# Optimization experiments

Hardware: AMD Instinct MI355X
Metric: run time of the kernel (lower is better)

## Reference

```python
import jax, jax.numpy as jnp
import numpy as np
import math

# Single graph (batch vector identically 0): per-graph topk and global_max_pool
# reduce to static lax.top_k and jnp.max. Pooled edge_index from SAGPooling is
# discarded because KnnEdges rebuilds the graph every layer (no_op=False).
N = 20000      # nodes
HID = 128      # in_channels == hidden_channels
L = 3          # num_layers
RATIO = 0.5    # pool_ratio
K0, KINC = 6, 2  # KnnEdges start_k / k_increment
OUT = 5


def setup_inputs() -> dict:
    key = jax.random.key(0)
    ks = jax.random.split(key, 10)
    s = 0.05  # keep tanh scores unsaturated
    x = jax.random.normal(ks[0], (N, HID), jnp.float32)
    pos = jax.random.uniform(ks[1], (N, 2), jnp.float32) * 100.0
    src = jax.random.randint(ks[2], (N * K0,), 0, N)
    dst = jnp.repeat(jnp.arange(N), K0)
    edge_index = jnp.stack([src, dst]).astype(jnp.int32)  # [2, E], row0=src(j), row1=dst(i)
    return dict(
        x=x, pos=pos, edge_index=edge_index,
        Wrel=jax.random.normal(ks[3], (L, HID, HID), jnp.float32) * s,
        brel=jnp.zeros((L, HID), jnp.float32),
        Wroot=jax.random.normal(ks[4], (L, HID, HID), jnp.float32) * s,
        Wprel=jax.random.normal(ks[5], (L, HID), jnp.float32) * s,
        bprel=jnp.zeros((L,), jnp.float32),
        Wproot=jax.random.normal(ks[6], (L, HID), jnp.float32) * s,
        W1=jax.random.normal(ks[7], (HID * L, HID), jnp.float32) * s,
        b1=jnp.zeros((HID,), jnp.float32),
        W2=jax.random.normal(ks[8], (HID, OUT), jnp.float32) * s,
        b2=jnp.zeros((OUT,), jnp.float32),
    )


def _mean_agg(x, src, dst, n):
    # mean over incoming messages x_j for each target i (PyG aggr='mean'; 0 if isolated)
    ssum = jax.ops.segment_sum(x[src], dst, num_segments=n)
    deg = jax.ops.segment_sum(jnp.ones(src.shape, x.dtype), dst, num_segments=n)
    return ssum / jnp.maximum(deg, 1.0)[:, None]


def reference(x, pos, edge_index, Wrel, brel, Wroot, Wprel, bprel, Wproot, W1, b1, W2, b2):
    src, dst = edge_index[0], edge_index[1]
    n = x.shape[0]
    xs = []
    for i in range(L):
        # GraphConv(aggr='mean'): out_i = W_rel @ mean_j x_j + W_root @ x_i + b
        agg = _mean_agg(x, src, dst, n)
        x = jax.nn.relu(agg @ Wrel[i] + x @ Wroot[i] + brel[i])
        # SAGPooling: score GNN = GraphConv(hid->1, aggr='add'); tanh nonlinearity
        sagg = jax.ops.segment_sum(x[src], dst, num_segments=n)
        score = jnp.tanh(sagg @ Wprel[i] + x @ Wproot[i] + bprel[i])  # [n]
        k_keep = math.ceil(RATIO * n)
        vals, perm = jax.lax.top_k(score, k_keep)
        x = x[perm] * vals[:, None]
        xs.append(jnp.max(x, axis=0))  # global_max_pool (single graph)
        # KnnEdges: pos = pos[perm]; rebuild KNN graph with k = start_k + i*k_increment
        pos = pos[perm]
        n = k_keep
        k = K0 + KINC * i
        d2 = jnp.sum((pos[:, None, :] - pos[None, :, :]) ** 2, axis=-1)  # [n, n]
        d2 = jnp.where(jnp.eye(n, dtype=bool), jnp.inf, d2)  # loop=False
        _, nbr = jax.lax.top_k(-d2, k)  # [n, k] nearest neighbors
        src = nbr.reshape(-1)                 # neighbor j (source)
        dst = jnp.repeat(jnp.arange(n), k)    # query i (target)
    h = jnp.concatenate(xs)  # JumpingKnowledge mode='cat' -> [HID*L]
    h = jax.nn.relu(h @ W1 + b1)  # dropout p=0.5 in eval mode: identity
    return (h @ W2 + b2)[None, :]  # [1, OUT]
```

## Files before the change

### kernel.cpp

```cpp
#include <hip/hip_runtime.h>
#include <hip/hip_bf16.h>
#include <math.h>

#define HID 128
#define PR 20
#define CRPB 32
#define CAND_CAP 8192
#define MAXCELLS 4096

__device__ inline int wave_iscan(int v, int lane) {
#pragma unroll
  for (int off = 1; off < 64; off <<= 1) {
    int o = __shfl_up(v, off, 64);
    if (lane >= off) v += o;
  }
  return v;
}

template <int K>
__global__ __launch_bounds__(256) void k_conv_fused(
    const float* __restrict__ x, const int* __restrict__ src, int n, float invk,
    const float* __restrict__ Wrel, const float* __restrict__ Wroot,
    const float* __restrict__ brel,
    const float* __restrict__ wprel, const float* __restrict__ wproot,
    float* __restrict__ out, float* __restrict__ uo, float* __restrict__ vo) {
  __shared__ float4 sagg4[CRPB][HID / 4];
  __shared__ float4 sx4[CRPB][HID / 4];
  __shared__ int ssrc[CRPB * K];
  int t = threadIdx.x;
  int i0 = blockIdx.x * CRPB;
  const int nK = n * K;
  for (int s = t; s < CRPB * K; s += 256) {
    int gi = i0 * K + s;
    int v = (gi < nK) ? src[gi] : 0;
    ssrc[s] = ((unsigned)v < (unsigned)n) ? v : 0;
  }
  __syncthreads();
  {
    int fq = t & 31, h = t >> 5;
    const float4* x4 = (const float4*)x;
    for (int r = h; r < CRPB; r += 8) {
      int row = i0 + r;
      float4 s = make_float4(0.f, 0.f, 0.f, 0.f);
      float4 xv = make_float4(0.f, 0.f, 0.f, 0.f);
      if (row < n) {
#pragma unroll
        for (int j = 0; j < K; ++j) {
          float4 xx = x4[(size_t)ssrc[r * K + j] * 32 + fq];
          s.x += xx.x; s.y += xx.y; s.z += xx.z; s.w += xx.w;
        }
        xv = x4[(size_t)row * 32 + fq];
      }
      s.x *= invk; s.y *= invk; s.z *= invk; s.w *= invk;
      sagg4[r][fq] = s;
      sx4[r][fq] = xv;
    }
  }
  __syncthreads();
  int q = t & 31, rg = t >> 5;
  const float4* Wrel4  = (const float4*)Wrel;
  const float4* Wroot4 = (const float4*)Wroot;
  float4 bq = ((const float4*)brel)[q];
  float4 acc[4];
#pragma unroll
  for (int rr = 0; rr < 4; ++rr) acc[rr] = bq;
  int rbase = rg * 4;
#pragma unroll 2
  for (int cq = 0; cq < HID / 4; ++cq) {
    float4 w1[4], w2[4];
#pragma unroll
    for (int uu = 0; uu < 4; ++uu) {
      w1[uu] = Wrel4[(cq * 4 + uu) * 32 + q];
      w2[uu] = Wroot4[(cq * 4 + uu) * 32 + q];
    }
#pragma unroll
    for (int rr = 0; rr < 4; ++rr) {
      float4 a  = sagg4[rbase + rr][cq];
      float4 xx = sx4[rbase + rr][cq];
      acc[rr].x += a.x*w1[0].x + a.y*w1[1].x + a.z*w1[2].x + a.w*w1[3].x
                 + xx.x*w2[0].x + xx.y*w2[1].x + xx.z*w2[2].x + xx.w*w2[3].x;
      acc[rr].y += a.x*w1[0].y + a.y*w1[1].y + a.z*w1[2].y + a.w*w1[3].y
                 + xx.x*w2[0].y + xx.y*w2[1].y + xx.z*w2[2].y + xx.w*w2[3].y;
      acc[rr].z += a.x*w1[0].z + a.y*w1[1].z + a.z*w1[2].z + a.w*w1[3].z
                 + xx.x*w2[0].z + xx.y*w2[1].z + xx.z*w2[2].z + xx.w*w2[3].z;
      acc[rr].w += a.x*w1[0].w + a.y*w1[1].w + a.z*w1[2].w + a.w*w1[3].w
                 + xx.x*w2[0].w + xx.y*w2[1].w + xx.z*w2[2].w + xx.w*w2[3].w;
    }
  }
  float4 wplq = ((const float4*)wprel)[q];
  float4 wprq = ((const float4*)wproot)[q];
#pragma unroll
  for (int rr = 0; rr < 4; ++rr) {
    int row = i0 + rbase + rr;
    float4 v = acc[rr];
    v.x = v.x > 0.f ? v.x : 0.f;
    v.y = v.y > 0.f ? v.y : 0.f;
    v.z = v.z > 0.f ? v.z : 0.f;
    v.w = v.w > 0.f ? v.w : 0.f;
    float pu = 0.f, pv = 0.f;
    if (row < n) {
      ((float4*)out)[(size_t)row * 32 + q] = v;
      pu = v.x * wplq.x + v.y * wplq.y + v.z * wplq.z + v.w * wplq.w;
      pv = v.x * wprq.x + v.y * wprq.y + v.z * wprq.z + v.w * wprq.w;
    }
#pragma unroll
    for (int o = 16; o; o >>= 1) {
      pu += __shfl_down(pu, o, 32);
      pv += __shfl_down(pv, o, 32);
    }
    if (q == 0 && row < n) { uo[row] = pu; vo[row] = pv; }
  }
}

template <int K>
__global__ __launch_bounds__(256) void k_score_lite(
    const float* __restrict__ u, const float* __restrict__ v,
    const int* __restrict__ src, const float* __restrict__ bprel,
    int n, float* __restrict__ score, unsigned* __restrict__ key,
    unsigned* __restrict__ ghist) {
  __shared__ unsigned lh[1024];
  int t = threadIdx.x;
#pragma unroll
  for (int uu = 0; uu < 4; ++uu) lh[t + uu * 256] = 0u;
  __syncthreads();
  int i = blockIdx.x * 256 + t;
  if (i < n) {
    float s = v[i] + bprel[0];
#pragma unroll
    for (int j = 0; j < K; ++j) s += u[src[i * K + j]];
    float sc = tanhf(s);
    score[i] = sc;
    unsigned bb = __float_as_uint(sc);
    unsigned k2 = (bb & 0x80000000u) ? ~bb : (bb | 0x80000000u);
    key[i] = k2;
    atomicAdd(&lh[k2 >> 22], 1u);
  }
  __syncthreads();
#pragma unroll
  for (int uu = 0; uu < 4; ++uu) {
    unsigned vv = lh[t + uu * 256];
    if (vv) atomicAdd(&ghist[t + uu * 256], vv);
  }
}

__global__ __launch_bounds__(256) void k_collect(
    const unsigned* __restrict__ key, int n, int kk,
    const unsigned* __restrict__ ghist,
    unsigned* __restrict__ BA, unsigned long long* __restrict__ candbuf,
    int* __restrict__ candCnt) {
  __shared__ int wt[4];
  __shared__ unsigned shB, shAbove;
  int t = threadIdx.x;
  int lane = t & 63, wid = t >> 6;
  unsigned h[4]; int s = 0;
#pragma unroll
  for (int uu = 0; uu < 4; ++uu) { h[uu] = ghist[t * 4 + uu]; s += (int)h[uu]; }
  int is = wave_iscan(s, lane);
  if (lane == 63) wt[wid] = is;
  __syncthreads();
  int b = 0, tot = 0;
#pragma unroll
  for (int w2 = 0; w2 < 4; ++w2) { int ss = wt[w2]; if (w2 < wid) b += ss; tot += ss; }
  int c = b + is - s;
#pragma unroll
  for (int uu = 0; uu < 4; ++uu) {
    c += (int)h[uu];
    unsigned above_strict = (unsigned)(tot - c);
    unsigned above_incl = above_strict + h[uu];
    if (above_incl >= (unsigned)kk && above_strict < (unsigned)kk) {
      shB = (unsigned)(t * 4 + uu);
      shAbove = above_strict;
    }
  }
  __syncthreads();
  unsigned B = shB;
  if (blockIdx.x == 0 && t == 0) { BA[0] = B; BA[1] = shAbove; }
  int i = blockIdx.x * 256 + t;
  unsigned long long lmask = (1ull << lane) - 1ull;
  unsigned kv = (i < n) ? key[i] : 0u;
  bool m = (i < n) && ((kv >> 22) == B);
  unsigned long long mm = __ballot(m);
  if (mm) {
    int leader = (int)(__ffsll((long long)mm) - 1);
    int base = 0;
    if (lane == leader) base = atomicAdd(candCnt, (int)__popcll(mm));
    base = __shfl(base, leader, 64);
    if (m) {
      int p = base + (int)__popcll(mm & lmask);
      if (p < CAND_CAP) candbuf[p] = ((unsigned long long)kv << 32) | (unsigned)(~i);
    }
  }
}

__global__ __launch_bounds__(1024) void k_refine(
    const unsigned long long* __restrict__ candbuf, const int* __restrict__ candCnt,
    const unsigned* __restrict__ BA, int kk, unsigned long long* __restrict__ T64) {
  extern __shared__ unsigned long long cands[];
  __shared__ unsigned hist256[256];
  __shared__ unsigned long long sh_prefix;
  __shared__ unsigned sh_remain;
  __shared__ int wtB[4];
  int t = threadIdx.x;
  int lane = t & 63, wid = t >> 6;
  unsigned B = BA[0], above = BA[1];
  int cnt = *candCnt; if (cnt > CAND_CAP) cnt = CAND_CAP;
  for (int i = t; i < cnt; i += 1024) cands[i] = candbuf[i];
  if (t == 0) {
    sh_prefix = ((unsigned long long)B) << 54;
    sh_remain = (unsigned)(kk - (int)above);
  }
  __syncthreads();
  const int shifts[7] = {46, 38, 30, 22, 14, 6, 0};
  for (int p = 0; p < 7; ++p) {
    int shift = shifts[p];
    int bits = (p == 6) ? 6 : 8;
    unsigned mask = (1u << bits) - 1u;
    unsigned long long himask = (p == 0) ? (~0ull << 54)
                                         : (~0ull << (shifts[p - 1]));
    unsigned long long prefix = sh_prefix;
    unsigned rem = sh_remain;
    if (t < 256) hist256[t] = 0u;
    __syncthreads();
    for (int i = t; i < cnt; i += 1024) {
      unsigned long long cc = cands[i];
      if ((cc & himask) == prefix)
        atomicAdd(&hist256[(unsigned)((cc >> shift) & mask)], 1u);
    }
    __syncthreads();
    int hv = (t < 256) ? (int)hist256[t] : 0;
    int iv = wave_iscan(hv, lane);
    if (t < 256 && lane == 63) wtB[wid] = iv;
    __syncthreads();
    if (t < 256) {
      int b = 0, tot = 0;
#pragma unroll
      for (int w2 = 0; w2 < 4; ++w2) { int s = wtB[w2]; if (w2 < wid) b += s; tot += s; }
      unsigned val = (unsigned)(iv + b);
      unsigned sstrict = (unsigned)tot - val;
      if ((unsigned)t <= mask && sstrict < rem && sstrict + (unsigned)hv >= rem) {
        sh_prefix = prefix | ((unsigned long long)t << shift);
        sh_remain = rem - sstrict;
      }
    }
    __syncthreads();
  }
  if (t == 0) T64[0] = sh_prefix;
}

__global__ void k_sel(const unsigned* __restrict__ key, int n,
                      const unsigned long long* __restrict__ T64,
                      int* __restrict__ perm, int* __restrict__ cntSel) {
  int i = blockIdx.x * blockDim.x + threadIdx.x;
  int lane = threadIdx.x & 63;
  unsigned long long lmask = (1ull << lane) - 1ull;
  unsigned long long T = T64[0];
  bool g = false;
  if (i < n) {
    unsigned long long k64 = ((unsigned long long)key[i] << 32) | (unsigned)(~i);
    g = (k64 >= T);
  }
  unsigned long long mg = __ballot(g);
  if (mg) {
    int leader = (int)(__ffsll((long long)mg) - 1);
    int base = 0;
    if (lane == leader) base = atomicAdd(cntSel, (int)__popcll(mg));
    base = __shfl(base, leader, 64);
    if (g) perm[base + (int)__popcll(mg & lmask)] = i;
  }
}

template <int R>
__global__ __launch_bounds__(256) void k_pool_pmax(
    const float* __restrict__ x, const float* __restrict__ score,
    const int* __restrict__ perm, const float* __restrict__ pos_in,
    float* __restrict__ xout, float* __restrict__ pos_out, int store,
    float* __restrict__ pmax, int* __restrict__ counts, int Gg, float inv_w) {
  __shared__ float sm[2][HID];
  int f = threadIdx.x & 127;
  int half = threadIdx.x >> 7;
  int j0 = blockIdx.x * R;
  float mx = -1e30f;
  for (int r = half; r < R; r += 2) {
    int j = j0 + r;
    int node = perm[j];
    float v = score[node];
    float val = x[(size_t)node * HID + f] * v;
    if (store) {
      xout[(size_t)j * HID + f] = val;
      if (f == 0) {
        float px = pos_in[node * 2], py = pos_in[node * 2 + 1];
        pos_out[j * 2] = px; pos_out[j * 2 + 1] = py;
        int cx = min(Gg - 1, max(0, (int)(px * inv_w)));
        int cy = min(Gg - 1, max(0, (int)(py * inv_w)));
        atomicAdd(&counts[cy * Gg + cx], 1);
      }
    }
    mx = fmaxf(mx, val);
  }
  sm[half][f] = mx;
  __syncthreads();
  if (half == 0) pmax[blockIdx.x * HID + f] = fmaxf(sm[0][f], sm[1][f]);
}

__global__ __launch_bounds__(256) void k_scatterF(
    const float2* __restrict__ pos, int m, int Gg, int cells, float inv_w,
    const int* __restrict__ counts, int* __restrict__ startsg, int* __restrict__ zcur,
    float2* __restrict__ spos, int* __restrict__ sidx) {
  __shared__ int sstarts[MAXCELLS];
  __shared__ int wsum[4];
  int t = threadIdx.x;
  int lane = t & 63, wid = t >> 6;
  int base16 = t * 16;
  int c0[16]; int s = 0;
#pragma unroll
  for (int u = 0; u < 16; ++u) {
    int idx = base16 + u;
    c0[u] = (idx < cells) ? counts[idx] : 0;
    s += c0[u];
  }
  int is = wave_iscan(s, lane);
  if (lane == 63) wsum[wid] = is;
  __syncthreads();
  int b = 0;
#pragma unroll
  for (int w2 = 0; w2 < 4; ++w2) { if (w2 < wid) b += wsum[w2]; }
  int excl = b + is - s;
#pragma unroll
  for (int u = 0; u < 16; ++u) {
    int idx = base16 + u;
    if (idx < cells) { sstarts[idx] = excl; excl += c0[u]; }
  }
  __syncthreads();
  if (blockIdx.x == 0) {
    for (int c = t; c < cells; c += 256) startsg[c] = sstarts[c];
  }
  int i = blockIdx.x * 256 + t;
  if (i < m) {
    float2 p = pos[i];
    int cx = min(Gg - 1, max(0, (int)(p.x * inv_w)));
    int cy = min(Gg - 1, max(0, (int)(p.y * inv_w)));
    int cell = cy * Gg + cx;
    int pp = sstarts[cell] + atomicAdd(&zcur[cell], 1);
    spos[pp] = p;
    sidx[pp] = i;
  }
}

template <int K>
__global__ __launch_bounds__(256) void k_knn_wave(const float2* __restrict__ spos,
                           const int* __restrict__ sidx,
                           const int* __restrict__ starts, const int* __restrict__ counts,
                           int m, int G, float w, float inv_w, int* __restrict__ src_out) {
  int lane = threadIdx.x & 63;
  int j = blockIdx.x * (blockDim.x >> 6) + (threadIdx.x >> 6);
  if (j >= m) return;
  float2 qp = spos[j];
  int q = sidx[j];
  int cx = min(G - 1, max(0, (int)(qp.x * inv_w)));
  int cy = min(G - 1, max(0, (int)(qp.y * inv_w)));

  float bd[K]; int bi[K];
#pragma unroll
  for (int t = 0; t < K; ++t) { bd[t] = 1e30f; bi[t] = 0; }

  auto scan_span = [&](int s, int e) {
    for (int p = s + lane; p < e; p += 64) {
      if (p == j) continue;
      float2 pp = spos[p];
      float dx = qp.x - pp.x, dy = qp.y - pp.y;
      float d = dx * dx + dy * dy;
      if (d < bd[K - 1]) {
        float dd = d; int ii = sidx[p];
#pragma unroll
        for (int t = 0; t < K; ++t) {
          bool sw = dd < bd[t];
          float od = bd[t]; int oi = bi[t];
          if (sw) { bd[t] = dd; bi[t] = ii; dd = od; ii = oi; }
        }
      }
    }
  };

  {
    int xl = max(0, cx - 1), xh = min(G - 1, cx + 1);
    int y0 = max(0, cy - 1), y1 = min(G - 1, cy + 1);
    int ss[3], ee[3]; int nr = 0;
    for (int y = y0; y <= y1; ++y) {
      int b = y * G;
      ss[nr] = starts[b + xl];
      ee[nr] = starts[b + xh] + counts[b + xh];
      ++nr;
    }
    for (int t = 0; t < nr; ++t) scan_span(ss[t], ee[t]);
  }

  int r = 1;
  unsigned long long mg[K];
  while (true) {
    unsigned long long tmp[K];
#pragma unroll
    for (int t = 0; t < K; ++t)
      tmp[t] = ((unsigned long long)__float_as_uint(bd[t]) << 32) | (unsigned)bi[t];
#pragma unroll
    for (int t = 0; t < K; ++t) {
      unsigned long long mn = tmp[0];
#pragma unroll
      for (int o = 1; o < 64; o <<= 1) {
        unsigned long long ot = __shfl_xor(mn, o, 64);
        if (ot < mn) mn = ot;
      }
      mg[t] = mn;
      if (tmp[0] == mn) {
#pragma unroll
        for (int s2 = 0; s2 < K - 1; ++s2) tmp[s2] = tmp[s2 + 1];
        tmp[K - 1] = ~0ull;
      }
    }
    float kth = __uint_as_float((unsigned)(mg[K - 1] >> 32));
    float bnd = 1e30f;
    if (cx - r > 0)     bnd = fminf(bnd, qp.x - (float)(cx - r) * w);
    if (cx + r < G - 1) bnd = fminf(bnd, (float)(cx + r + 1) * w - qp.x);
    if (cy - r > 0)     bnd = fminf(bnd, qp.y - (float)(cy - r) * w);
    if (cy + r < G - 1) bnd = fminf(bnd, (float)(cy + r + 1) * w - qp.y);
    if (bnd > 1e29f) break;
    float bb = fmaxf(bnd, 0.f) * 0.999f;
    if (kth < bb * bb) break;
    ++r;
    int xl = max(0, cx - r), xh = min(G - 1, cx + r);
    int yt = cy - r, yb = cy + r;
    if (yt >= 0)     { int b = yt * G; scan_span(starts[b + xl], starts[b + xh] + counts[b + xh]); }
    if (yb <= G - 1) { int b = yb * G; scan_span(starts[b + xl], starts[b + xh] + counts[b + xh]); }
    int ylo = max(0, cy - r + 1), yhi = min(G - 1, cy + r - 1);
    for (int y = ylo; y <= yhi; ++y) {
      int b = y * G;
      if (cx - r >= 0)     { int c = b + cx - r; scan_span(starts[c], starts[c] + counts[c]); }
      if (cx + r <= G - 1) { int c = b + cx + r; scan_span(starts[c], starts[c] + counts[c]); }
    }
  }
  if (lane == 0) {
#pragma unroll
    for (int t = 0; t < K; ++t) src_out[q * K + t] = (int)(unsigned)(mg[t] & 0xffffffffu);
  }
}

__global__ __launch_bounds__(256) void k_colmax2(const float* __restrict__ pmax,
                                                 int P0, int P1, int P2,
                                                 float* __restrict__ pmax2) {
  __shared__ float sm[2][HID];
  int l = blockIdx.x >> 3, c = blockIdx.x & 7;
  int lo3[3] = {0, P0, P0 + P1};
  int len3[3] = {P0, P1, P2};
  int lo = lo3[l], len = len3[l];
  int f = threadIdx.x & 127, half = threadIdx.x >> 7;
  float mx = -1e30f;
  for (int p = c + 8 * half; p < len; p += 16)
    mx = fmaxf(mx, pmax[(size_t)(lo + p) * HID + f]);
  sm[half][f] = mx;
  __syncthreads();
  if (half == 0) pmax2[(size_t)blockIdx.x * HID + f] = fmaxf(sm[0][f], sm[1][f]);
}

__global__ __launch_bounds__(1024) void k_final(const float* __restrict__ pmax2,
                        const float* __restrict__ W1, const float* __restrict__ b1,
                        const float* __restrict__ W2, const float* __restrict__ b2,
                        float* __restrict__ out) {
  __shared__ float sxs[3 * HID];
  __shared__ float red[8][HID];
  __shared__ float h1[HID];
  int f = threadIdx.x & 127, ch = threadIdx.x >> 7;
  if (ch < 3) {
    float mx = pmax2[(size_t)(ch * 8) * HID + f];
#pragma unroll
    for (int u = 1; u < 8; ++u) mx = fmaxf(mx, pmax2[(size_t)(ch * 8 + u) * HID + f]);
    sxs[ch * HID + f] = mx;
  }
  __syncthreads();
  float acc = 0.f;
  for (int c = ch * 48; c < (ch + 1) * 48; ++c) acc += sxs[c] * W1[c * HID + f];
  red[ch][f] = acc;
  __syncthreads();
  if (ch == 0) {
    float a = b1[f];
#pragma unroll
    for (int u = 0; u < 8; ++u) a += red[u][f];
    h1[f] = a > 0.f ? a : 0.f;
  }
  __syncthreads();
  if (threadIdx.x < 5) {
    float a = b2[threadIdx.x];
    for (int c = 0; c < HID; ++c) a += h1[c] * W2[c * 5 + threadIdx.x];
    out[threadIdx.x] = a;
  }
}

extern "C" void kernel_launch(void* const* d_in, const int* in_sizes, int n_in,
                              void* d_out, int out_size, void* d_ws, size_t ws_size,
                              hipStream_t stream) {
  const float* x_in   = (const float*)d_in[0];
  const float* pos_in = (const float*)d_in[1];
  const int*   ei     = (const int*)d_in[2];
  const float* Wrel   = (const float*)d_in[3];
  const float* brel   = (const float*)d_in[4];
  const float* Wroot  = (const float*)d_in[5];
  const float* Wprel  = (const float*)d_in[6];
  const float* bprel  = (const float*)d_in[7];
  const float* Wproot = (const float*)d_in[8];
  const float* W1     = (const float*)d_in[9];
  const float* b1     = (const float*)d_in[10];
  const float* W2     = (const float*)d_in[11];
  const float* b2     = (const float*)d_in[12];
  float* out = (float*)d_out;

  const int N0 = in_sizes[0] / HID;
  const int P0 = (N0 / 2) / PR, P1 = (N0 / 4) / PR, P2 = (N0 / 8) / PR;

  char* w = (char*)d_ws;
  float*    xB     = (float*)w;    w += (size_t)N0 * HID * 4;
  float*    xA     = (float*)w;    w += (size_t)(N0 / 2) * HID * 4;
  float*    score  = (float*)w;    w += (size_t)N0 * 4;
  unsigned* key    = (unsigned*)w; w += (size_t)N0 * 4;
  float*    ubuf   = (float*)w;    w += (size_t)N0 * 4;
  float*    vbuf   = (float*)w;    w += (size_t)N0 * 4;
  float*    posA   = (float*)w;    w += (size_t)(N0 / 2) * 2 * 4;
  float*    posB   = (float*)w;    w += (size_t)(N0 / 2) * 2 * 4;
  int*      srcbuf = (int*)w;      w += (size_t)(N0 / 2) * 8 * 4;
  int*      permb  = (int*)w;      w += (size_t)(N0 / 2) * 4;
  float*    pmax   = (float*)w;    w += (size_t)(P0 + P1 + P2) * HID * 4;
  float*    pmax2  = (float*)w;    w += (size_t)24 * HID * 4;
  unsigned* ghistB = (unsigned*)w; w += 3 * 1024 * 4;
  int*      cnt    = (int*)w;      w += 16 * 4;
  int*      countsB= (int*)w;      w += 2 * MAXCELLS * 4;
  int*      zcurB  = (int*)w;      w += 2 * MAXCELLS * 4;
  const size_t ZERO_BYTES = 3 * 1024 * 4 + 16 * 4 + 4 * MAXCELLS * 4;
  unsigned long long* T64 = (unsigned long long*)w; w += 16;
  unsigned* BA     = (unsigned*)w; w += 16;
  unsigned long long* candbuf = (unsigned long long*)w; w += CAND_CAP * 8;
  int*      starts = (int*)w;      w += MAXCELLS * 4;
  float2*   spos   = (float2*)w;   w += (size_t)(N0 / 2) * 8;
  int*      sidx   = (int*)w;      w += (size_t)(N0 / 2) * 4;
  (void)ws_size; (void)n_in; (void)out_size;

  hipMemsetAsync(ghistB, 0, ZERO_BYTES, stream);

  int n = N0;
  const float* xcur   = x_in;
  const float* poscur = pos_in;
  const int*   srccur = ei;
  int kcur = 6;
  int Poff = 0;

  for (int l = 0; l < 3; ++l) {
    const int kk = n / 2;
    int Gg = (int)ceilf(sqrtf((float)kk / 2.5f));
    if (Gg > 64) Gg = 64;
    if (Gg < 1) Gg = 1;
    int cells = Gg * Gg;
    float cw = 100.f / (float)Gg;
    float inv_w = (float)Gg / 100.f;
    int cblocks = (n + CRPB - 1) / CRPB;
    int sblocks = (n + 255) / 256;
    unsigned* ghist = ghistB + l * 1024;
    int* counts = countsB + (l < 2 ? l : 0) * MAXCELLS;
    int* zcur   = zcurB + (l < 2 ? l : 0) * MAXCELLS;

    if (kcur == 6) {
      k_conv_fused<6><<<cblocks, 256, 0, stream>>>(xcur, srccur, n, 1.f / 6.f,
          Wrel + l * HID * HID, Wroot + l * HID * HID, brel + l * HID,
          Wprel + l * HID, Wproot + l * HID, xB, ubuf, vbuf);
      k_score_lite<6><<<sblocks, 256, 0, stream>>>(ubuf, vbuf, srccur, bprel + l,
                                                   n, score, key, ghist);
    } else {
      k_conv_fused<8><<<cblocks, 256, 0, stream>>>(xcur, srccur, n, 1.f / 8.f,
          Wrel + l * HID * HID, Wroot + l * HID * HID, brel + l * HID,
          Wprel + l * HID, Wproot + l * HID, xB, ubuf, vbuf);
      k_score_lite<8><<<sblocks, 256, 0, stream>>>(ubuf, vbuf, srccur, bprel + l,
                                                   n, score, key, ghist);
    }
    k_collect<<<sblocks, 256, 0, stream>>>(key, n, kk, ghist, BA, candbuf, cnt + 2 * l);
    k_refine<<<1, 1024, CAND_CAP * 8, stream>>>(candbuf, cnt + 2 * l, BA, kk, T64);
    k_sel<<<sblocks, 256, 0, stream>>>(key, n, T64, permb, cnt + 2 * l + 1);

    float* pos_out = (l == 0) ? posA : posB;
    int store = (l < 2) ? 1 : 0;
    k_pool_pmax<PR><<<kk / PR, 256, 0, stream>>>(xB, score, permb, poscur, xA, pos_out,
                                                 store, pmax + (size_t)Poff * HID,
                                                 counts, Gg, inv_w);
    Poff += kk / PR;
    n = kk;
    if (l < 2) {
      k_scatterF<<<(n + 255) / 256, 256, 0, stream>>>((const float2*)pos_out, n, Gg, cells,
                                                      inv_w, counts, starts, zcur, spos, sidx);
      if (l == 0) { k_knn_wave<6><<<(n + 3) / 4, 256, 0, stream>>>(spos, sidx, starts, counts,
                                                                   n, Gg, cw, inv_w, srcbuf); kcur = 6; }
      else        { k_knn_wave<8><<<(n + 3) / 4, 256, 0, stream>>>(spos, sidx, starts, counts,
                                                                   n, Gg, cw, inv_w, srcbuf); kcur = 8; }
    }
    xcur = xA; poscur = pos_out; srccur = srcbuf;
  }
  k_colmax2<<<24, 256, 0, stream>>>(pmax, P0, P1, P2, pmax2);
  k_final<<<1, 1024, 0, stream>>>(pmax2, W1, b1, W2, b2, out);
}
```

Before: 244.5 us.

## Split fused conv into dense dual GEMM then neighbor gather of projected features

```diff
diff --git a/kernel.cpp b/kernel.cpp
--- a/kernel.cpp
+++ b/kernel.cpp
@@ -4,7 +4,6 @@
 
 #define HID 128
 #define PR 20
-#define CRPB 32
 #define CAND_CAP 8192
 #define MAXCELLS 4096
 
@@ -17,53 +16,31 @@
   return v;
 }
 
-template <int K>
-__global__ __launch_bounds__(256) void k_conv_fused(
-    const float* __restrict__ x, const int* __restrict__ src, int n, float invk,
+__global__ __launch_bounds__(256) void k_gemm2(
+    const float* __restrict__ x, int n,
     const float* __restrict__ Wrel, const float* __restrict__ Wroot,
-    const float* __restrict__ brel,
-    const float* __restrict__ wprel, const float* __restrict__ wproot,
-    float* __restrict__ out, float* __restrict__ uo, float* __restrict__ vo) {
-  __shared__ float4 sagg4[CRPB][HID / 4];
-  __shared__ float4 sx4[CRPB][HID / 4];
-  __shared__ int ssrc[CRPB * K];
+    float* __restrict__ Y, float* __restrict__ Z) {
+  __shared__ float4 sx4[32][HID / 4];
   int t = threadIdx.x;
-  int i0 = blockIdx.x * CRPB;
-  const int nK = n * K;
-  for (int s = t; s < CRPB * K; s += 256) {
-    int gi = i0 * K + s;
-    int v = (gi < nK) ? src[gi] : 0;
-    ssrc[s] = ((unsigned)v < (unsigned)n) ? v : 0;
-  }
-  __syncthreads();
+  int i0 = blockIdx.x * 32;
   {
     int fq = t & 31, h = t >> 5;
     const float4* x4 = (const float4*)x;
-    for (int r = h; r < CRPB; r += 8) {
+    for (int r = h; r < 32; r += 8) {
       int row = i0 + r;
-      float4 s = make_float4(0.f, 0.f, 0.f, 0.f);
-      float4 xv = make_float4(0.f, 0.f, 0.f, 0.f);
-      if (row < n) {
-#pragma unroll
-        for (int j = 0; j < K; ++j) {
-          float4 xx = x4[(size_t)ssrc[r * K + j] * 32 + fq];
-          s.x += xx.x; s.y += xx.y; s.z += xx.z; s.w += xx.w;
-        }
-        xv = x4[(size_t)row * 32 + fq];
-      }
-      s.x *= invk; s.y *= invk; s.z *= invk; s.w *= invk;
-      sagg4[r][fq] = s;
-      sx4[r][fq] = xv;
+      sx4[r][fq] = (row < n) ? x4[(size_t)row * 32 + fq] : make_float4(0.f, 0.f, 0.f, 0.f);
     }
   }
   __syncthreads();
   int q = t & 31, rg = t >> 5;
   const float4* Wrel4  = (const float4*)Wrel;
   const float4* Wroot4 = (const float4*)Wroot;
-  float4 bq = ((const float4*)brel)[q];
-  float4 acc[4];
-#pragma unroll
-  for (int rr = 0; rr < 4; ++rr) acc[rr] = bq;
+  float4 accY[4], accZ[4];
+#pragma unroll
+  for (int rr = 0; rr < 4; ++rr) {
+    accY[rr] = make_float4(0.f, 0.f, 0.f, 0.f);
+    accZ[rr] = make_float4(0.f, 0.f, 0.f, 0.f);
+  }
   int rbase = rg * 4;
 #pragma unroll 2
   for (int cq = 0; cq < HID / 4; ++cq) {
@@ -75,40 +52,78 @@
     }
 #pragma unroll
     for (int rr = 0; rr < 4; ++rr) {
-      float4 a  = sagg4[rbase + rr][cq];
       float4 xx = sx4[rbase + rr][cq];
-      acc[rr].x += a.x*w1[0].x + a.y*w1[1].x + a.z*w1[2].x + a.w*w1[3].x
-                 + xx.x*w2[0].x + xx.y*w2[1].x + xx.z*w2[2].x + xx.w*w2[3].x;
-      acc[rr].y += a.x*w1[0].y + a.y*w1[1].y + a.z*w1[2].y + a.w*w1[3].y
-                 + xx.x*w2[0].y + xx.y*w2[1].y + xx.z*w2[2].y + xx.w*w2[3].y;
-      acc[rr].z += a.x*w1[0].z + a.y*w1[1].z + a.z*w1[2].z + a.w*w1[3].z
-                 + xx.x*w2[0].z + xx.y*w2[1].z + xx.z*w2[2].z + xx.w*w2[3].z;
-      acc[rr].w += a.x*w1[0].w + a.y*w1[1].w + a.z*w1[2].w + a.w*w1[3].w
-                 + xx.x*w2[0].w + xx.y*w2[1].w + xx.z*w2[2].w + xx.w*w2[3].w;
-    }
-  }
-  float4 wplq = ((const float4*)wprel)[q];
-  float4 wprq = ((const float4*)wproot)[q];
+      accY[rr].x += xx.x*w1[0].x + xx.y*w1[1].x + xx.z*w1[2].x + xx.w*w1[3].x;
+      accY[rr].y += xx.x*w1[0].y + xx.y*w1[1].y + xx.z*w1[2].y + xx.w*w1[3].y;
+      accY[rr].z += xx.x*w1[0].z + xx.y*w1[1].z + xx.z*w1[2].z + xx.w*w1[3].z;
+      accY[rr].w += xx.x*w1[0].w + xx.y*w1[1].w + xx.z*w1[2].w + xx.w*w1[3].w;
+      accZ[rr].x += xx.x*w2[0].x + xx.y*w2[1].x + xx.z*w2[2].x + xx.w*w2[3].x;
+      accZ[rr].y += xx.x*w2[0].y + xx.y*w2[1].y + xx.z*w2[2].y + xx.w*w2[3].y;
+      accZ[rr].z += xx.x*w2[0].z + xx.y*w2[1].z + xx.z*w2[2].z + xx.w*w2[3].z;
+      accZ[rr].w += xx.x*w2[0].w + xx.y*w2[1].w + xx.z*w2[2].w + xx.w*w2[3].w;
+    }
+  }
 #pragma unroll
   for (int rr = 0; rr < 4; ++rr) {
     int row = i0 + rbase + rr;
-    float4 v = acc[rr];
+    if (row < n) {
+      ((float4*)Y)[(size_t)row * 32 + q] = accY[rr];
+      ((float4*)Z)[(size_t)row * 32 + q] = accZ[rr];
+    }
+  }
+}
+
+template <int K>
+__global__ __launch_bounds__(256) void k_gatherout(
+    const float* __restrict__ Y, const float* __restrict__ Z,
+    const int* __restrict__ src, int n, float invk,
+    const float* __restrict__ brel,
+    const float* __restrict__ wprel, const float* __restrict__ wproot,
+    float* __restrict__ out, float* __restrict__ uo, float* __restrict__ vo) {
+  __shared__ int ssrc[16 * K];
+  int t = threadIdx.x;
+  int i0 = blockIdx.x * 16;
+  const int nK = n * K;
+  if (t < 16 * K) {
+    int gi = i0 * K + t;
+    int v = (gi < nK) ? src[gi] : 0;
+    ssrc[t] = ((unsigned)v < (unsigned)n) ? v : 0;
+  }
+  __syncthreads();
+  int fq = t & 31, h = t >> 5;
+  const float4* Y4 = (const float4*)Y;
+  const float4* Z4 = (const float4*)Z;
+  float4 bq   = ((const float4*)brel)[fq];
+  float4 wplq = ((const float4*)wprel)[fq];
+  float4 wprq = ((const float4*)wproot)[fq];
+  for (int r = h; r < 16; r += 8) {
+    int row = i0 + r;
+    if (row >= n) continue;
+    float4 s = make_float4(0.f, 0.f, 0.f, 0.f);
+#pragma unroll
+    for (int j = 0; j < K; ++j) {
+      float4 yy = Y4[(size_t)ssrc[r * K + j] * 32 + fq];
+      s.x += yy.x; s.y += yy.y; s.z += yy.z; s.w += yy.w;
+    }
+    float4 z = Z4[(size_t)row * 32 + fq];
+    float4 v;
+    v.x = s.x * invk + z.x + bq.x;
+    v.y = s.y * invk + z.y + bq.y;
+    v.z = s.z * invk + z.z + bq.z;
+    v.w = s.w * invk + z.w + bq.w;
     v.x = v.x > 0.f ? v.x : 0.f;
     v.y = v.y > 0.f ? v.y : 0.f;
     v.z = v.z > 0.f ? v.z : 0.f;
     v.w = v.w > 0.f ? v.w : 0.f;
-    float pu = 0.f, pv = 0.f;
-    if (row < n) {
-      ((float4*)out)[(size_t)row * 32 + q] = v;
-      pu = v.x * wplq.x + v.y * wplq.y + v.z * wplq.z + v.w * wplq.w;
-      pv = v.x * wprq.x + v.y * wprq.y + v.z * wprq.z + v.w * wprq.w;
-    }
+    ((float4*)out)[(size_t)row * 32 + fq] = v;
+    float pu = v.x * wplq.x + v.y * wplq.y + v.z * wplq.z + v.w * wplq.w;
+    float pv = v.x * wprq.x + v.y * wprq.y + v.z * wprq.z + v.w * wprq.w;
 #pragma unroll
     for (int o = 16; o; o >>= 1) {
       pu += __shfl_down(pu, o, 32);
       pv += __shfl_down(pv, o, 32);
     }
-    if (q == 0 && row < n) { uo[row] = pu; vo[row] = pv; }
+    if (fq == 0) { uo[row] = pu; vo[row] = pv; }
   }
 }
 
@@ -516,6 +531,8 @@
 
   char* w = (char*)d_ws;
   float*    xB     = (float*)w;    w += (size_t)N0 * HID * 4;
+  float*    Ybuf   = (float*)w;    w += (size_t)N0 * HID * 4;
+  float*    Zbuf   = (float*)w;    w += (size_t)N0 * HID * 4;
   float*    xA     = (float*)w;    w += (size_t)(N0 / 2) * HID * 4;
   float*    score  = (float*)w;    w += (size_t)N0 * 4;
   unsigned* key    = (unsigned*)w; w += (size_t)N0 * 4;
@@ -557,22 +574,23 @@
     int cells = Gg * Gg;
     float cw = 100.f / (float)Gg;
     float inv_w = (float)Gg / 100.f;
-    int cblocks = (n + CRPB - 1) / CRPB;
+    int gblocks = (n + 31) / 32;
+    int goblocks = (n + 15) / 16;
     int sblocks = (n + 255) / 256;
     unsigned* ghist = ghistB + l * 1024;
     int* counts = countsB + (l < 2 ? l : 0) * MAXCELLS;
     int* zcur   = zcurB + (l < 2 ? l : 0) * MAXCELLS;
 
+    k_gemm2<<<gblocks, 256, 0, stream>>>(xcur, n, Wrel + l * HID * HID,
+                                         Wroot + l * HID * HID, Ybuf, Zbuf);
     if (kcur == 6) {
-      k_conv_fused<6><<<cblocks, 256, 0, stream>>>(xcur, srccur, n, 1.f / 6.f,
-          Wrel + l * HID * HID, Wroot + l * HID * HID, brel + l * HID,
-          Wprel + l * HID, Wproot + l * HID, xB, ubuf, vbuf);
+      k_gatherout<6><<<goblocks, 256, 0, stream>>>(Ybuf, Zbuf, srccur, n, 1.f / 6.f,
+          brel + l * HID, Wprel + l * HID, Wproot + l * HID, xB, ubuf, vbuf);
       k_score_lite<6><<<sblocks, 256, 0, stream>>>(ubuf, vbuf, srccur, bprel + l,
                                                    n, score, key, ghist);
     } else {
-      k_conv_fused<8><<<cblocks, 256, 0, stream>>>(xcur, srccur, n, 1.f / 8.f,
-          Wrel + l * HID * HID, Wroot + l * HID * HID, brel + l * HID,
-          Wprel + l * HID, Wproot + l * HID, xB, ubuf, vbuf);
+      k_gatherout<8><<<goblocks, 256, 0, stream>>>(Ybuf, Zbuf, srccur, n, 1.f / 8.f,
+          brel + l * HID, Wprel + l * HID, Wproot + l * HID, xB, ubuf, vbuf);
       k_score_lite<8><<<sblocks, 256, 0, stream>>>(ubuf, vbuf, srccur, bprel + l,
                                                    n, score, key, ghist);
     }
```

Result: slower. 274.0 us (+12.0%).

## Store pooled nodes in spatial-cell order to drop index remapping

Applied to the files above, without the earlier changes.

```diff
diff --git a/kernel.cpp b/kernel.cpp
--- a/kernel.cpp
+++ b/kernel.cpp
@@ -249,7 +249,9 @@
 
 __global__ void k_sel(const unsigned* __restrict__ key, int n,
                       const unsigned long long* __restrict__ T64,
-                      int* __restrict__ perm, int* __restrict__ cntSel) {
+                      int* __restrict__ perm, int* __restrict__ cntSel,
+                      const float* __restrict__ pos_prev, int* __restrict__ counts,
+                      int Gg, float inv_w, int docount) {
   int i = blockIdx.x * blockDim.x + threadIdx.x;
   int lane = threadIdx.x & 63;
   unsigned long long lmask = (1ull << lane) - 1ull;
@@ -267,14 +269,65 @@
     base = __shfl(base, leader, 64);
     if (g) perm[base + (int)__popcll(mg & lmask)] = i;
   }
+  if (g && docount) {
+    float px = pos_prev[i * 2], py = pos_prev[i * 2 + 1];
+    int cx = min(Gg - 1, max(0, (int)(px * inv_w)));
+    int cy = min(Gg - 1, max(0, (int)(py * inv_w)));
+    atomicAdd(&counts[cy * Gg + cx], 1);
+  }
+}
+
+__global__ __launch_bounds__(256) void k_scatterS(
+    const int* __restrict__ perm, int kk, const float* __restrict__ pos_prev,
+    int Gg, int cells, float inv_w,
+    const int* __restrict__ counts, int* __restrict__ startsg, int* __restrict__ zcur,
+    float2* __restrict__ spos, int* __restrict__ snode) {
+  __shared__ int sstarts[MAXCELLS];
+  __shared__ int wsum[4];
+  int t = threadIdx.x;
+  int lane = t & 63, wid = t >> 6;
+  int base16 = t * 16;
+  int c0[16]; int s = 0;
+#pragma unroll
+  for (int u = 0; u < 16; ++u) {
+    int idx = base16 + u;
+    c0[u] = (idx < cells) ? counts[idx] : 0;
+    s += c0[u];
+  }
+  int is = wave_iscan(s, lane);
+  if (lane == 63) wsum[wid] = is;
+  __syncthreads();
+  int b = 0;
+#pragma unroll
+  for (int w2 = 0; w2 < 4; ++w2) { if (w2 < wid) b += wsum[w2]; }
+  int excl = b + is - s;
+#pragma unroll
+  for (int u = 0; u < 16; ++u) {
+    int idx = base16 + u;
+    if (idx < cells) { sstarts[idx] = excl; excl += c0[u]; }
+  }
+  __syncthreads();
+  if (blockIdx.x == 0) {
+    for (int c = t; c < cells; c += 256) startsg[c] = sstarts[c];
+  }
+  int j = blockIdx.x * 256 + t;
+  if (j < kk) {
+    int node = perm[j];
+    float px = pos_prev[node * 2], py = pos_prev[node * 2 + 1];
+    int cx = min(Gg - 1, max(0, (int)(px * inv_w)));
+    int cy = min(Gg - 1, max(0, (int)(py * inv_w)));
+    int cell = cy * Gg + cx;
+    int pp = sstarts[cell] + atomicAdd(&zcur[cell], 1);
+    spos[pp] = make_float2(px, py);
+    snode[pp] = node;
+  }
 }
 
 template <int R>
 __global__ __launch_bounds__(256) void k_pool_pmax(
     const float* __restrict__ x, const float* __restrict__ score,
-    const int* __restrict__ perm, const float* __restrict__ pos_in,
-    float* __restrict__ xout, float* __restrict__ pos_out, int store,
-    float* __restrict__ pmax, int* __restrict__ counts, int Gg, float inv_w) {
+    const int* __restrict__ snode,
+    float* __restrict__ xout, int store, float* __restrict__ pmax) {
   __shared__ float sm[2][HID];
   int f = threadIdx.x & 127;
   int half = threadIdx.x >> 7;
@@ -282,80 +335,25 @@
   float mx = -1e30f;
   for (int r = half; r < R; r += 2) {
     int j = j0 + r;
-    int node = perm[j];
+    int node = snode[j];
     float v = score[node];
     float val = x[(size_t)node * HID + f] * v;
-    if (store) {
-      xout[(size_t)j * HID + f] = val;
-      if (f == 0) {
-        float px = pos_in[node * 2], py = pos_in[node * 2 + 1];
-        pos_out[j * 2] = px; pos_out[j * 2 + 1] = py;
-        int cx = min(Gg - 1, max(0, (int)(px * inv_w)));
-        int cy = min(Gg - 1, max(0, (int)(py * inv_w)));
-        atomicAdd(&counts[cy * Gg + cx], 1);
-      }
-    }
+    if (store) xout[(size_t)j * HID + f] = val;
     mx = fmaxf(mx, val);
   }
   sm[half][f] = mx;
   __syncthreads();
   if (half == 0) pmax[blockIdx.x * HID + f] = fmaxf(sm[0][f], sm[1][f]);
-}
-
-__global__ __launch_bounds__(256) void k_scatterF(
-    const float2* __restrict__ pos, int m, int Gg, int cells, float inv_w,
-    const int* __restrict__ counts, int* __restrict__ startsg, int* __restrict__ zcur,
-    float2* __restrict__ spos, int* __restrict__ sidx) {
-  __shared__ int sstarts[MAXCELLS];
-  __shared__ int wsum[4];
-  int t = threadIdx.x;
-  int lane = t & 63, wid = t >> 6;
-  int base16 = t * 16;
-  int c0[16]; int s = 0;
-#pragma unroll
-  for (int u = 0; u < 16; ++u) {
-    int idx = base16 + u;
-    c0[u] = (idx < cells) ? counts[idx] : 0;
-    s += c0[u];
-  }
-  int is = wave_iscan(s, lane);
-  if (lane == 63) wsum[wid] = is;
-  __syncthreads();
-  int b = 0;
-#pragma unroll
-  for (int w2 = 0; w2 < 4; ++w2) { if (w2 < wid) b += wsum[w2]; }
-  int excl = b + is - s;
-#pragma unroll
-  for (int u = 0; u < 16; ++u) {
-    int idx = base16 + u;
-    if (idx < cells) { sstarts[idx] = excl; excl += c0[u]; }
-  }
-  __syncthreads();
-  if (blockIdx.x == 0) {
-    for (int c = t; c < cells; c += 256) startsg[c] = sstarts[c];
-  }
-  int i = blockIdx.x * 256 + t;
-  if (i < m) {
-    float2 p = pos[i];
-    int cx = min(Gg - 1, max(0, (int)(p.x * inv_w)));
-    int cy = min(Gg - 1, max(0, (int)(p.y * inv_w)));
-    int cell = cy * Gg + cx;
-    int pp = sstarts[cell] + atomicAdd(&zcur[cell], 1);
-    spos[pp] = p;
-    sidx[pp] = i;
-  }
 }
 
 template <int K>
 __global__ __launch_bounds__(256) void k_knn_wave(const float2* __restrict__ spos,
-                           const int* __restrict__ sidx,
                            const int* __restrict__ starts, const int* __restrict__ counts,
                            int m, int G, float w, float inv_w, int* __restrict__ src_out) {
   int lane = threadIdx.x & 63;
   int j = blockIdx.x * (blockDim.x >> 6) + (threadIdx.x >> 6);
   if (j >= m) return;
   float2 qp = spos[j];
-  int q = sidx[j];
   int cx = min(G - 1, max(0, (int)(qp.x * inv_w)));
   int cy = min(G - 1, max(0, (int)(qp.y * inv_w)));
 
@@ -370,7 +368,7 @@
       float dx = qp.x - pp.x, dy = qp.y - pp.y;
       float d = dx * dx + dy * dy;
       if (d < bd[K - 1]) {
-        float dd = d; int ii = sidx[p];
+        float dd = d; int ii = p;
 #pragma unroll
         for (int t = 0; t < K; ++t) {
           bool sw = dd < bd[t];
@@ -439,7 +437,7 @@
   }
   if (lane == 0) {
 #pragma unroll
-    for (int t = 0; t < K; ++t) src_out[q * K + t] = (int)(unsigned)(mg[t] & 0xffffffffu);
+    for (int t = 0; t < K; ++t) src_out[j * K + t] = (int)(unsigned)(mg[t] & 0xffffffffu);
   }
 }
 
@@ -521,10 +519,11 @@
   unsigned* key    = (unsigned*)w; w += (size_t)N0 * 4;
   float*    ubuf   = (float*)w;    w += (size_t)N0 * 4;
   float*    vbuf   = (float*)w;    w += (size_t)N0 * 4;
-  float*    posA   = (float*)w;    w += (size_t)(N0 / 2) * 2 * 4;
-  float*    posB   = (float*)w;    w += (size_t)(N0 / 2) * 2 * 4;
   int*      srcbuf = (int*)w;      w += (size_t)(N0 / 2) * 8 * 4;
   int*      permb  = (int*)w;      w += (size_t)(N0 / 2) * 4;
+  int*      snode  = (int*)w;      w += (size_t)(N0 / 2) * 4;
+  float2*   sposA  = (float2*)w;   w += (size_t)(N0 / 2) * 8;
+  float2*   sposB  = (float2*)w;   w += (size_t)(N0 / 2) * 8;
   float*    pmax   = (float*)w;    w += (size_t)(P0 + P1 + P2) * HID * 4;
   float*    pmax2  = (float*)w;    w += (size_t)24 * HID * 4;
   unsigned* ghistB = (unsigned*)w; w += 3 * 1024 * 4;
@@ -536,8 +535,6 @@
   unsigned* BA     = (unsigned*)w; w += 16;
   unsigned long long* candbuf = (unsigned long long*)w; w += CAND_CAP * 8;
   int*      starts = (int*)w;      w += MAXCELLS * 4;
-  float2*   spos   = (float2*)w;   w += (size_t)(N0 / 2) * 8;
-  int*      sidx   = (int*)w;      w += (size_t)(N0 / 2) * 4;
   (void)ws_size; (void)n_in; (void)out_size;
 
   hipMemsetAsync(ghistB, 0, ZERO_BYTES, stream);
@@ -546,7 +543,6 @@
   const float* xcur   = x_in;
   const float* poscur = pos_in;
   const int*   srccur = ei;
-  int kcur = 6;
   int Poff = 0;
 
   for (int l = 0; l < 3; ++l) {
@@ -557,20 +553,19 @@
     int cells = Gg * Gg;
     float cw = 100.f / (float)Gg;
     float inv_w = (float)Gg / 100.f;
-    int cblocks = (n + CRPB - 1) / CRPB;
     int sblocks = (n + 255) / 256;
     unsigned* ghist = ghistB + l * 1024;
     int* counts = countsB + (l < 2 ? l : 0) * MAXCELLS;
     int* zcur   = zcurB + (l < 2 ? l : 0) * MAXCELLS;
 
-    if (kcur == 6) {
-      k_conv_fused<6><<<cblocks, 256, 0, stream>>>(xcur, srccur, n, 1.f / 6.f,
+    if (l < 2) {
+      k_conv_fused<6><<<(n + CRPB - 1) / CRPB, 256, 0, stream>>>(xcur, srccur, n, 1.f / 6.f,
           Wrel + l * HID * HID, Wroot + l * HID * HID, brel + l * HID,
           Wprel + l * HID, Wproot + l * HID, xB, ubuf, vbuf);
       k_score_lite<6><<<sblocks, 256, 0, stream>>>(ubuf, vbuf, srccur, bprel + l,
                                                    n, score, key, ghist);
     } else {
-      k_conv_fused<8><<<cblocks, 256, 0, stream>>>(xcur, srccur, n, 1.f / 8.f,
+      k_conv_fused<8><<<(n + CRPB - 1) / CRPB, 256, 0, stream>>>(xcur, srccur, n, 1.f / 8.f,
           Wrel + l * HID * HID, Wroot + l * HID * HID, brel + l * HID,
           Wprel + l * HID, Wproot + l * HID, xB, ubuf, vbuf);
       k_score_lite<8><<<sblocks, 256, 0, stream>>>(ubuf, vbuf, srccur, bprel + l,
@@ -578,24 +573,29 @@
     }
     k_collect<<<sblocks, 256, 0, stream>>>(key, n, kk, ghist, BA, candbuf, cnt + 2 * l);
     k_refine<<<1, 1024, CAND_CAP * 8, stream>>>(candbuf, cnt + 2 * l, BA, kk, T64);
-    k_sel<<<sblocks, 256, 0, stream>>>(key, n, T64, permb, cnt + 2 * l + 1);
-
-    float* pos_out = (l == 0) ? posA : posB;
+    k_sel<<<sblocks, 256, 0, stream>>>(key, n, T64, permb, cnt + 2 * l + 1,
+                                       poscur, counts, Gg, inv_w, (l < 2) ? 1 : 0);
+
+    float2* sposL = (l == 0) ? sposA : sposB;
     int store = (l < 2) ? 1 : 0;
-    k_pool_pmax<PR><<<kk / PR, 256, 0, stream>>>(xB, score, permb, poscur, xA, pos_out,
-                                                 store, pmax + (size_t)Poff * HID,
-                                                 counts, Gg, inv_w);
+    const int* poolmap = permb;
+    if (l < 2) {
+      k_scatterS<<<(kk + 255) / 256, 256, 0, stream>>>(permb, kk, poscur, Gg, cells, inv_w,
+                                                       counts, starts, zcur, sposL, snode);
+      poolmap = snode;
+    }
+    k_pool_pmax<PR><<<kk / PR, 256, 0, stream>>>(xB, score, poolmap, xA, store,
+                                                 pmax + (size_t)Poff * HID);
     Poff += kk / PR;
     n = kk;
-    if (l < 2) {
-      k_scatterF<<<(n + 255) / 256, 256, 0, stream>>>((const float2*)pos_out, n, Gg, cells,
-                                                      inv_w, counts, starts, zcur, spos, sidx);
-      if (l == 0) { k_knn_wave<6><<<(n + 3) / 4, 256, 0, stream>>>(spos, sidx, starts, counts,
-                                                                   n, Gg, cw, inv_w, srcbuf); kcur = 6; }
-      else        { k_knn_wave<8><<<(n + 3) / 4, 256, 0, stream>>>(spos, sidx, starts, counts,
-                                                                   n, Gg, cw, inv_w, srcbuf); kcur = 8; }
-    }
-    xcur = xA; poscur = pos_out; srccur = srcbuf;
+    if (l == 0) {
+      k_knn_wave<6><<<(n + 3) / 4, 256, 0, stream>>>(sposL, starts, counts,
+                                                     n, Gg, cw, inv_w, srcbuf);
+    } else if (l == 1) {
+      k_knn_wave<8><<<(n + 3) / 4, 256, 0, stream>>>(sposL, starts, counts,
+                                                     n, Gg, cw, inv_w, srcbuf);
+    }
+    xcur = xA; poscur = (const float*)sposL; srccur = srcbuf;
   }
   k_colmax2<<<24, 256, 0, stream>>>(pmax, P0, P1, P2, pmax2);
   k_final<<<1, 1024, 0, stream>>>(pmax2, W1, b1, W2, b2, out);
```

Measured after the change: 235.8 us, median of 2. -3.6%, faster.
